# Kernel tuning notes

Measured on AMD Instinct MI355X. Metric: run time of the kernel, lower is better.

The kernel has to match this reference:

```python
import jax, jax.numpy as jnp
import numpy as np

N = 100000
E = 625000
IN_C, HID_C, OUT_C = 128, 128, 128


def setup_inputs() -> dict:
    key = jax.random.key(0)
    ks = jax.random.split(key, 8)
    x = jax.random.normal(ks[0], (N, IN_C), dtype=jnp.float32)
    edge_index = jax.random.randint(ks[1], (2, E), 0, N, dtype=jnp.int64)
    # SAGEConv layer 1: lin_l (on aggregated neighbors, with bias), lin_r (on root, no bias)
    s1 = 1.0 / np.sqrt(IN_C)
    W1l = jax.random.uniform(ks[2], (HID_C, IN_C), minval=-s1, maxval=s1, dtype=jnp.float32)
    b1l = jax.random.uniform(ks[3], (HID_C,), minval=-s1, maxval=s1, dtype=jnp.float32)
    W1r = jax.random.uniform(ks[4], (HID_C, IN_C), minval=-s1, maxval=s1, dtype=jnp.float32)
    s2 = 1.0 / np.sqrt(HID_C)
    W2l = jax.random.uniform(ks[5], (OUT_C, HID_C), minval=-s2, maxval=s2, dtype=jnp.float32)
    b2l = jax.random.uniform(ks[6], (OUT_C,), minval=-s2, maxval=s2, dtype=jnp.float32)
    W2r = jax.random.uniform(ks[7], (OUT_C, HID_C), minval=-s2, maxval=s2, dtype=jnp.float32)
    return {"x": x, "edge_index": edge_index,
            "W1l": W1l, "b1l": b1l, "W1r": W1r,
            "W2l": W2l, "b2l": b2l, "W2r": W2r}


def _sage_conv(x, src, dst, Wl, bl, Wr, num_nodes):
    # mean aggregation of source features into destination nodes
    agg = jax.ops.segment_sum(x[src], dst, num_segments=num_nodes)  # [N, d]
    cnt = jax.ops.segment_sum(jnp.ones((src.shape[0],), dtype=x.dtype), dst,
                              num_segments=num_nodes)  # [N]
    mean = agg / jnp.maximum(cnt, 1.0)[:, None]  # zero-degree nodes stay 0
    return mean @ Wl.T + bl + x @ Wr.T


def reference(x, edge_index, W1l, b1l, W1r, W2l, b2l, W2r):
    src, dst = edge_index[0], edge_index[1]
    h = jax.nn.sigmoid(_sage_conv(x, src, dst, W1l, b1l, W1r, N))
    out = _sage_conv(h, src, dst, W2l, b2l, W2r, N)
    return out
```

## Files before the change

kernel.cpp:

```cpp
#include <hip/hip_runtime.h>
#include <math.h>

#define NN 100000
#define NE 625000
#define CC 128
#define CAP 32
#define NT2 1563
#define LSTR 264

typedef __attribute__((ext_vector_type(8))) short bf16x8;
typedef __attribute__((ext_vector_type(4))) float f32x4;

__device__ __forceinline__ unsigned short f2b(float f) {
    unsigned int u = __float_as_uint(f);
    unsigned int r = (u + 0x7FFFu + ((u >> 16) & 1u)) >> 16;
    return (unsigned short)r;
}
__device__ __forceinline__ float b2f(unsigned int h) {
    return __uint_as_float(h << 16);
}


__global__ void build_kernel(const int* __restrict__ src, const int* __restrict__ dst,
                             int* __restrict__ cnt, int* __restrict__ col) {
    int e = blockIdx.x * blockDim.x + threadIdx.x;
    if (e < NE) {
        int d = dst[e];
        int p = atomicAdd(&cnt[d], 1);
        if (p < CAP) col[d * CAP + p] = src[e];
    }
}


__global__ __launch_bounds__(256) void cvtX_kernel(const float* __restrict__ x,
                                                   unsigned short* __restrict__ xb) {
    size_t i = ((size_t)blockIdx.x * 256 + threadIdx.x) * 4;
    float4 v = *(const float4*)&x[i];
    ushort2 lo = { f2b(v.x), f2b(v.y) };
    ushort2 hi = { f2b(v.z), f2b(v.w) };
    *(ushort2*)&xb[i]     = lo;
    *(ushort2*)&xb[i + 2] = hi;
}


__global__ void cvtW_kernel(const float* __restrict__ W1l, const float* __restrict__ W1r,
                            const float* __restrict__ W2l, const float* __restrict__ W2r,
                            unsigned short* __restrict__ Wcat1,
                            unsigned short* __restrict__ Wcat2) {
    int i = blockIdx.x * blockDim.x + threadIdx.x;
    int layer = i >> 15;
    int local = i & 32767;
    int c = local >> 8;
    int k = local & 255;
    const float* Wl = layer ? W2l : W1l;
    const float* Wr = layer ? W2r : W1r;
    float v = (k < CC) ? Wl[c * CC + k] : Wr[c * CC + (k - CC)];
    (layer ? Wcat2 : Wcat1)[local] = f2b(v);
}


__global__ __launch_bounds__(256) void gather_kernel(const unsigned short* __restrict__ feat,
                                                     const int* __restrict__ cnt,
                                                     const int* __restrict__ col,
                                                     unsigned short* __restrict__ aggb) {
    int gtid = blockIdx.x * blockDim.x + threadIdx.x;
    int node = gtid >> 6;
    if (node >= NN) return;
    int lane = gtid & 63;
    int g    = lane >> 4;
    int c8   = (lane & 15) * 8;
    int deg  = cnt[node];
    int dmin = deg < CAP ? deg : CAP;
    const int* bucket = col + node * CAP;
    float s0 = 0, s1 = 0, s2 = 0, s3 = 0, s4 = 0, s5 = 0, s6 = 0, s7 = 0;
    for (int j = g; j < dmin; j += 4) {
        int s = bucket[j];
        uint4 u = *(const uint4*)&feat[(size_t)s * CC + c8];
        s0 += b2f(u.x & 0xFFFFu); s1 += b2f(u.x >> 16);
        s2 += b2f(u.y & 0xFFFFu); s3 += b2f(u.y >> 16);
        s4 += b2f(u.z & 0xFFFFu); s5 += b2f(u.z >> 16);
        s6 += b2f(u.w & 0xFFFFu); s7 += b2f(u.w >> 16);
    }
    s0 += __shfl_xor(s0, 16); s0 += __shfl_xor(s0, 32);
    s1 += __shfl_xor(s1, 16); s1 += __shfl_xor(s1, 32);
    s2 += __shfl_xor(s2, 16); s2 += __shfl_xor(s2, 32);
    s3 += __shfl_xor(s3, 16); s3 += __shfl_xor(s3, 32);
    s4 += __shfl_xor(s4, 16); s4 += __shfl_xor(s4, 32);
    s5 += __shfl_xor(s5, 16); s5 += __shfl_xor(s5, 32);
    s6 += __shfl_xor(s6, 16); s6 += __shfl_xor(s6, 32);
    s7 += __shfl_xor(s7, 16); s7 += __shfl_xor(s7, 32);
    if (g == 0) {
        float iv = 1.0f / (float)(deg > 0 ? deg : 1);
        uint4 o;
        o.x = (unsigned int)f2b(s0 * iv) | ((unsigned int)f2b(s1 * iv) << 16);
        o.y = (unsigned int)f2b(s2 * iv) | ((unsigned int)f2b(s3 * iv) << 16);
        o.z = (unsigned int)f2b(s4 * iv) | ((unsigned int)f2b(s5 * iv) << 16);
        o.w = (unsigned int)f2b(s6 * iv) | ((unsigned int)f2b(s7 * iv) << 16);
        *(uint4*)&aggb[(size_t)node * CC + c8] = o;
    }
}


template<bool SIGMOID, bool OUT_FP32>
__global__ __launch_bounds__(256, 3) void gemm3_kernel(
        const unsigned short* __restrict__ aggb,
        const unsigned short* __restrict__ featb,
        const unsigned short* __restrict__ Wcat,
        const float* __restrict__ bias,
        void* __restrict__ outv) {
    __shared__ unsigned short Acat[64 * LSTR];

    const int t    = threadIdx.x;
    const int w    = t >> 6;
    const int lane = t & 63;
    const int m    = lane & 15;
    const int kq   = lane >> 4;
    const int col0 = w * 32;

    bf16x8 breg[2][8];
#pragma unroll
    for (int ct = 0; ct < 2; ++ct)
#pragma unroll
        for (int ks = 0; ks < 8; ++ks)
            breg[ct][ks] = *(const bf16x8*)(Wcat + (size_t)(col0 + ct * 16 + m) * 256 + ks * 32 + kq * 8);

    const float bias0 = bias[col0 + m];
    const float bias1 = bias[col0 + 16 + m];

    const int sr  = t >> 2;
    const int seg = t & 3;

    for (int rt = blockIdx.x; rt < NT2; rt += gridDim.x) {
        const int row0 = rt * 64;

        int gr = row0 + sr; if (gr >= NN) gr = NN - 1;
        const unsigned short* srcp = (seg < 2)
            ? (aggb  + (size_t)gr * CC + seg * 64)
            : (featb + (size_t)gr * CC + (seg - 2) * 64);
        bf16x8 st[8];
#pragma unroll
        for (int j = 0; j < 8; ++j) st[j] = *(const bf16x8*)(srcp + j * 8);

        __syncthreads();

        unsigned short* q = &Acat[sr * LSTR + seg * 64];
#pragma unroll
        for (int j = 0; j < 8; ++j) *(bf16x8*)(q + j * 8) = st[j];

        __syncthreads();

        f32x4 acc[4][2];
#pragma unroll
        for (int rt4 = 0; rt4 < 4; ++rt4)
#pragma unroll
            for (int ct = 0; ct < 2; ++ct) acc[rt4][ct] = (f32x4)0.0f;

#pragma unroll
        for (int ks = 0; ks < 8; ++ks) {
            bf16x8 a[4];
#pragma unroll
            for (int rt4 = 0; rt4 < 4; ++rt4)
                a[rt4] = *(const bf16x8*)&Acat[(rt4 * 16 + m) * LSTR + ks * 32 + kq * 8];
#pragma unroll
            for (int rt4 = 0; rt4 < 4; ++rt4) {
                acc[rt4][0] = __builtin_amdgcn_mfma_f32_16x16x32_bf16(a[rt4], breg[0][ks], acc[rt4][0], 0, 0, 0);
                acc[rt4][1] = __builtin_amdgcn_mfma_f32_16x16x32_bf16(a[rt4], breg[1][ks], acc[rt4][1], 0, 0, 0);
            }
        }

#pragma unroll
        for (int rt4 = 0; rt4 < 4; ++rt4) {
#pragma unroll
            for (int ct = 0; ct < 2; ++ct) {
                const int c = col0 + ct * 16 + m;
                const float bv = ct ? bias1 : bias0;
#pragma unroll
                for (int i = 0; i < 4; ++i) {
                    const int r = row0 + rt4 * 16 + kq * 4 + i;
                    if (r < NN) {
                        float v = acc[rt4][ct][i] + bv;
                        if (SIGMOID) v = 1.0f / (1.0f + __expf(-v));
                        if (OUT_FP32) ((float*)outv)[(size_t)r * CC + c] = v;
                        else ((unsigned short*)outv)[(size_t)r * CC + c] = f2b(v);
                    }
                }
            }
        }
    }
}


extern "C" void kernel_launch(void* const* d_in, const int* in_sizes, int n_in,
                              void* d_out, int out_size, void* d_ws, size_t ws_size,
                              hipStream_t stream) {
    const float* x   = (const float*)d_in[0];
    const int*   ei  = (const int*)d_in[1];
    const float* W1l = (const float*)d_in[2];
    const float* b1l = (const float*)d_in[3];
    const float* W1r = (const float*)d_in[4];
    const float* W2l = (const float*)d_in[5];
    const float* b2l = (const float*)d_in[6];
    const float* W2r = (const float*)d_in[7];
    float* out = (float*)d_out;

    const int* src = ei;
    const int* dst = ei + NE;

    int* cnt = (int*)d_ws;
    int* col = cnt + NN;
    unsigned short* Wcat1 = (unsigned short*)(col + NN * CAP);
    unsigned short* Wcat2 = Wcat1 + 128 * 256;
    unsigned short* xb    = Wcat2 + 128 * 256;
    unsigned short* aggb  = xb + (size_t)NN * CC;
    unsigned short* hb    = aggb + (size_t)NN * CC;

    hipMemsetAsync(cnt, 0, (size_t)NN * sizeof(int), stream);

    build_kernel<<<(NE + 255) / 256, 256, 0, stream>>>(src, dst, cnt, col);
    cvtX_kernel<<<(NN * CC / 4) / 256, 256, 0, stream>>>(x, xb);
    cvtW_kernel<<<256, 256, 0, stream>>>(W1l, W1r, W2l, W2r, Wcat1, Wcat2);

    const int GB = 1024;

    gather_kernel<<<(NN * 64) / 256, 256, 0, stream>>>(xb, cnt, col, aggb);
    gemm3_kernel<true, false><<<GB, 256, 0, stream>>>(aggb, xb, Wcat1, b1l, hb);

    gather_kernel<<<(NN * 64) / 256, 256, 0, stream>>>(hb, cnt, col, aggb);
    gemm3_kernel<false, true><<<GB, 256, 0, stream>>>(aggb, hb, Wcat2, b2l, out);
}
```

Baseline: 274.3 us.

## Gather with 16 lanes per node and 4-way unrolled masked neighbor loads

The gather kernel now maps one node to 16 lanes instead of 64, so each lane walks every neighbor rather than a quarter of them. The cross-group shuffle reduction goes away. The loop is unrolled by four with clamped indices and 0/1 masks, which puts four independent 16-byte loads in flight per iteration. The GEMM grid also changes from 1024 to 782 blocks. The trade is less parallelism per node and some redundant loads on padded iterations, in exchange for more memory-level parallelism per thread and no reduction overhead.

```diff
diff --git a/kernel.cpp b/kernel.cpp
--- a/kernel.cpp
+++ b/kernel.cpp
@@ -59,45 +59,50 @@
 }
 
 
+#define ACC8(u, m) \
+    s0 = fmaf(m, b2f((u).x & 0xFFFFu), s0); s1 = fmaf(m, b2f((u).x >> 16), s1); \
+    s2 = fmaf(m, b2f((u).y & 0xFFFFu), s2); s3 = fmaf(m, b2f((u).y >> 16), s3); \
+    s4 = fmaf(m, b2f((u).z & 0xFFFFu), s4); s5 = fmaf(m, b2f((u).z >> 16), s5); \
+    s6 = fmaf(m, b2f((u).w & 0xFFFFu), s6); s7 = fmaf(m, b2f((u).w >> 16), s7);
+
 __global__ __launch_bounds__(256) void gather_kernel(const unsigned short* __restrict__ feat,
                                                      const int* __restrict__ cnt,
                                                      const int* __restrict__ col,
                                                      unsigned short* __restrict__ aggb) {
     int gtid = blockIdx.x * blockDim.x + threadIdx.x;
-    int node = gtid >> 6;
+    int node = gtid >> 4;
     if (node >= NN) return;
-    int lane = gtid & 63;
-    int g    = lane >> 4;
-    int c8   = (lane & 15) * 8;
-    int deg  = cnt[node];
+    int c8 = (gtid & 15) * 8;
+    int deg = cnt[node];
     int dmin = deg < CAP ? deg : CAP;
-    const int* bucket = col + node * CAP;
+    const int* __restrict__ bucket = col + node * CAP;
     float s0 = 0, s1 = 0, s2 = 0, s3 = 0, s4 = 0, s5 = 0, s6 = 0, s7 = 0;
-    for (int j = g; j < dmin; j += 4) {
-        int s = bucket[j];
-        uint4 u = *(const uint4*)&feat[(size_t)s * CC + c8];
-        s0 += b2f(u.x & 0xFFFFu); s1 += b2f(u.x >> 16);
-        s2 += b2f(u.y & 0xFFFFu); s3 += b2f(u.y >> 16);
-        s4 += b2f(u.z & 0xFFFFu); s5 += b2f(u.z >> 16);
-        s6 += b2f(u.w & 0xFFFFu); s7 += b2f(u.w >> 16);
+    int dpad = (dmin + 3) & ~3;
+    for (int j = 0; j < dpad; j += 4) {
+        int i1 = j + 1, i2 = j + 2, i3 = j + 3;
+        float m1 = i1 < dmin ? 1.0f : 0.0f;
+        float m2 = i2 < dmin ? 1.0f : 0.0f;
+        float m3 = i3 < dmin ? 1.0f : 0.0f;
+        if (i1 >= dmin) i1 = dmin - 1;
+        if (i2 >= dmin) i2 = dmin - 1;
+        if (i3 >= dmin) i3 = dmin - 1;
+        int n0 = bucket[j], n1 = bucket[i1], n2 = bucket[i2], n3 = bucket[i3];
+        uint4 u0 = *(const uint4*)&feat[(size_t)n0 * CC + c8];
+        uint4 u1 = *(const uint4*)&feat[(size_t)n1 * CC + c8];
+        uint4 u2 = *(const uint4*)&feat[(size_t)n2 * CC + c8];
+        uint4 u3 = *(const uint4*)&feat[(size_t)n3 * CC + c8];
+        ACC8(u0, 1.0f);
+        ACC8(u1, m1);
+        ACC8(u2, m2);
+        ACC8(u3, m3);
     }
-    s0 += __shfl_xor(s0, 16); s0 += __shfl_xor(s0, 32);
-    s1 += __shfl_xor(s1, 16); s1 += __shfl_xor(s1, 32);
-    s2 += __shfl_xor(s2, 16); s2 += __shfl_xor(s2, 32);
-    s3 += __shfl_xor(s3, 16); s3 += __shfl_xor(s3, 32);
-    s4 += __shfl_xor(s4, 16); s4 += __shfl_xor(s4, 32);
-    s5 += __shfl_xor(s5, 16); s5 += __shfl_xor(s5, 32);
-    s6 += __shfl_xor(s6, 16); s6 += __shfl_xor(s6, 32);
-    s7 += __shfl_xor(s7, 16); s7 += __shfl_xor(s7, 32);
-    if (g == 0) {
-        float iv = 1.0f / (float)(deg > 0 ? deg : 1);
-        uint4 o;
-        o.x = (unsigned int)f2b(s0 * iv) | ((unsigned int)f2b(s1 * iv) << 16);
-        o.y = (unsigned int)f2b(s2 * iv) | ((unsigned int)f2b(s3 * iv) << 16);
-        o.z = (unsigned int)f2b(s4 * iv) | ((unsigned int)f2b(s5 * iv) << 16);
-        o.w = (unsigned int)f2b(s6 * iv) | ((unsigned int)f2b(s7 * iv) << 16);
-        *(uint4*)&aggb[(size_t)node * CC + c8] = o;
-    }
+    float iv = 1.0f / (float)(deg > 0 ? deg : 1);
+    uint4 o;
+    o.x = (unsigned int)f2b(s0 * iv) | ((unsigned int)f2b(s1 * iv) << 16);
+    o.y = (unsigned int)f2b(s2 * iv) | ((unsigned int)f2b(s3 * iv) << 16);
+    o.z = (unsigned int)f2b(s4 * iv) | ((unsigned int)f2b(s5 * iv) << 16);
+    o.w = (unsigned int)f2b(s6 * iv) | ((unsigned int)f2b(s7 * iv) << 16);
+    *(uint4*)&aggb[(size_t)node * CC + c8] = o;
 }
 
 
@@ -220,11 +225,11 @@
     cvtX_kernel<<<(NN * CC / 4) / 256, 256, 0, stream>>>(x, xb);
     cvtW_kernel<<<256, 256, 0, stream>>>(W1l, W1r, W2l, W2r, Wcat1, Wcat2);
 
-    const int GB = 1024;
-
-    gather_kernel<<<(NN * 64) / 256, 256, 0, stream>>>(xb, cnt, col, aggb);
+    const int GB = 782;
+
+    gather_kernel<<<(NN * 16) / 256, 256, 0, stream>>>(xb, cnt, col, aggb);
     gemm3_kernel<true, false><<<GB, 256, 0, stream>>>(aggb, xb, Wcat1, b1l, hb);
 
-    gather_kernel<<<(NN * 64) / 256, 256, 0, stream>>>(hb, cnt, col, aggb);
+    gather_kernel<<<(NN * 16) / 256, 256, 0, stream>>>(hb, cnt, col, aggb);
     gemm3_kernel<false, true><<<GB, 256, 0, stream>>>(aggb, hb, Wcat2, b2l, out);
 }
```

New measurement: 252.5 us. -7.9%, faster.
